# Performance work log

Hardware: AMD Instinct MI355X
Metric: run time of the kernel (lower is better)

Reference implementation:

```python
import jax, jax.numpy as jnp
import numpy as np

# Instant-NGP HashGrid constants (match tcnn encoding_config defaults in the module)
N_LEVELS = 16
N_FEATS = 2
LOG2_T = 16
T = 1 << LOG2_T            # hashmap entries per level
BASE_RES = 16
PER_LEVEL_SCALE = 1.5
N_POINTS = 1 << 20
PRIMES = (1, 2654435761, 805459861)  # tcnn spatial-hash primes

# 8 corner offsets of the unit cube, [8,3]
_CORNERS = np.array([[i, j, k] for i in (0, 1) for j in (0, 1) for k in (0, 1)], dtype=np.float32)


def setup_inputs() -> dict:
    key = jax.random.key(0)
    k1, k2 = jax.random.split(key)
    x = jax.random.uniform(k1, (N_POINTS, 3), dtype=jnp.float32)
    # tcnn initializes hash tables uniform in [-1e-4, 1e-4]
    table = jax.random.uniform(k2, (N_LEVELS, T, N_FEATS), minval=-1e-4, maxval=1e-4, dtype=jnp.float32)
    return {"x": x, "table": table}


def _corner_index(grid, res, dense):
    # grid: [N,8,3] int32 corner coordinates -> [N,8] table index
    if dense:
        g = jnp.clip(grid, 0, res - 1)
        return g[..., 0] + g[..., 1] * res + g[..., 2] * res * res
    g = grid.astype(jnp.uint32)
    h = (g[..., 0] * jnp.uint32(PRIMES[0])
         ^ g[..., 1] * jnp.uint32(PRIMES[1])
         ^ g[..., 2] * jnp.uint32(PRIMES[2]))
    return (h & jnp.uint32(T - 1)).astype(jnp.int32)


def _hashgrid_forward(x, table):
    x = x.astype(jnp.float32)
    offs = jnp.asarray(_CORNERS)                      # [8,3]
    outs = []
    for level in range(N_LEVELS):
        # tcnn: grid_scale = base * s^level - 1 ; resolution = ceil(scale)+1
        scale = float(BASE_RES * (PER_LEVEL_SCALE ** level) - 1.0)
        res = int(np.ceil(scale)) + 1
        dense = res ** 3 <= T                          # tcnn uses dense indexing when the grid fits
        pos = x * scale + 0.5                          # [N,3]
        g0 = jnp.floor(pos)
        frac = pos - g0                                # [N,3] trilinear fractions
        grid = (g0[:, None, :] + offs[None]).astype(jnp.int32)   # [N,8,3]
        idx = _corner_index(grid, res, dense)          # [N,8]
        feat = table[level][idx]                       # [N,8,F] irregular gather
        # trilinear weights: prod over dims of frac or (1-frac) per corner
        w = jnp.prod(jnp.where(offs[None] > 0, frac[:, None, :], 1.0 - frac[:, None, :]), axis=-1)  # [N,8]
        outs.append(jnp.sum(w[..., None] * feat, axis=1))        # [N,F]
    return jnp.concatenate(outs, axis=-1)              # [N, L*F] = [N,32]


def reference(x, table):
    return _hashgrid_forward(x, table)
```

## Files before the change

kernel.cpp:

```cpp
#include <hip/hip_runtime.h>
#include <stdint.h>


#define NLVL 16
#define TS 65536
#define P2 2654435761u
#define P3 805459861u

typedef float v4f __attribute__((ext_vector_type(4)));
typedef float v2f __attribute__((ext_vector_type(2)));
typedef float v4fa8 __attribute__((ext_vector_type(4), aligned(8)));

__constant__ float C_SCALES[NLVL] = {
    15.0f, 23.0f, 35.0f, 53.0f, 80.0f, 120.5f, 181.25f, 272.375f,
    409.0625f, 614.09375f, 921.640625f, 1382.9609375f,
    2074.94140625f, 3112.912109375f, 4669.8681640625f, 7005.30224609375f};

__device__ __forceinline__ v2f v4lo8(v4fa8 v) { v2f r; r.x = v.x; r.y = v.y; return r; }
__device__ __forceinline__ v2f v4hi8(v4fa8 v) { v2f r; r.x = v.z; r.y = v.w; return r; }

__device__ __forceinline__ void lds_put2(float* s, int p, int l,
                                         float a, float b) {
    const int t = l >> 3;
    const int gl = (l >> 1) & 3;
    const int slot = (gl + p) & 3;
    const int a32 = t * 4096 + p * 16 + slot * 4 + (l & 1) * 2;
    s[a32] = a;
    s[a32 + 1] = b;
}

struct LvlS {
    v2f c0, c1, c2, c3, c4, c5, c6, c7;
    float wx, wy, wz;
};

__device__ __forceinline__ void lvl_issue(LvlS& s, float px, float py,
                                          float pz, float scale,
                                          const v2f* __restrict__ tbl) {
    const float fx = px * scale + 0.5f;
    const float fy = py * scale + 0.5f;
    const float fz = pz * scale + 0.5f;
    const float gx = floorf(fx), gy = floorf(fy), gz = floorf(fz);
    s.wx = fx - gx;
    s.wy = fy - gy;
    s.wz = fz - gz;
    const uint32_t bx = (uint32_t)(int)gx, bx1 = bx + 1;
    const uint32_t hy0 = (uint32_t)(int)gy * P2, hy1 = hy0 + P2;
    const uint32_t hz0 = (uint32_t)(int)gz * P3, hz1 = hz0 + P3;
    const uint32_t b00 = hy0 ^ hz0, b01 = hy0 ^ hz1;
    const uint32_t b10 = hy1 ^ hz0, b11 = hy1 ^ hz1;
    s.c0 = tbl[(bx ^ b00) & (TS - 1)];
    s.c1 = tbl[(bx ^ b01) & (TS - 1)];
    s.c2 = tbl[(bx ^ b10) & (TS - 1)];
    s.c3 = tbl[(bx ^ b11) & (TS - 1)];
    s.c4 = tbl[(bx1 ^ b00) & (TS - 1)];
    s.c5 = tbl[(bx1 ^ b01) & (TS - 1)];
    s.c6 = tbl[(bx1 ^ b10) & (TS - 1)];
    s.c7 = tbl[(bx1 ^ b11) & (TS - 1)];
}

__device__ __forceinline__ v2f lvl_consume(const LvlS& s) {
    const float ux = 1.0f - s.wx, uy = 1.0f - s.wy, uz = 1.0f - s.wz;
    const float w0 = ux * uy * uz, w1 = ux * uy * s.wz;
    const float w2 = ux * s.wy * uz, w3 = ux * s.wy * s.wz;
    const float w4 = s.wx * uy * uz, w5 = s.wx * uy * s.wz;
    const float w6 = s.wx * s.wy * uz, w7 = s.wx * s.wy * s.wz;
    v2f o;
    o.x = w0 * s.c0.x + w1 * s.c1.x + w2 * s.c2.x + w3 * s.c3.x +
          w4 * s.c4.x + w5 * s.c5.x + w6 * s.c6.x + w7 * s.c7.x;
    o.y = w0 * s.c0.y + w1 * s.c1.y + w2 * s.c2.y + w3 * s.c3.y +
          w4 * s.c4.y + w5 * s.c5.y + w6 * s.c6.y + w7 * s.c7.y;
    return o;
}

__global__ __launch_bounds__(256, 4) void hashgrid_fwd(
    const float* __restrict__ x,
    const float* __restrict__ table,
    float* __restrict__ out,
    int n)
{
    __shared__ float s_out[256 * 32];

    const int tid0 = blockIdx.x * 256 + threadIdx.x;
    const int tid = min(tid0, n - 1);
    const int p = threadIdx.x;

    const float px = x[3 * tid + 0];
    const float py = x[3 * tid + 1];
    const float pz = x[3 * tid + 2];

    v4f* outb4 = (v4f*)out + (size_t)blockIdx.x * (256 * 8);
    const long long lim4 = (long long)n * 8 - (long long)blockIdx.x * (256 * 8);

    const v2f* tblv = (const v2f*)table;

    LvlS s0, s1, s2;
    lvl_issue(s0, px, py, pz, C_SCALES[3], tblv + (size_t)3 * TS);
    lvl_issue(s1, px, py, pz, C_SCALES[4], tblv + (size_t)4 * TS);
    lvl_issue(s2, px, py, pz, C_SCALES[5], tblv + (size_t)5 * TS);

    {
        const int RESO[3] = {16, 24, 36};
        const float DSC[3] = {15.0f, 23.0f, 35.0f};
#pragma unroll
        for (int l = 0; l < 3; ++l) {
            const float scale = DSC[l];
            const float fx = px * scale + 0.5f;
            const float fy = py * scale + 0.5f;
            const float fz = pz * scale + 0.5f;
            const float gx = floorf(fx), gy = floorf(fy), gz = floorf(fz);
            const float wx = fx - gx, wy = fy - gy, wz = fz - gz;
            const int ix = (int)gx, iy = (int)gy, iz = (int)gz;

            const v2f* tbl = tblv + (size_t)l * TS;
            const int R = RESO[l];
            const int x0 = min(ix, R - 1);
            const int y0 = min(iy, R - 1), y1 = min(iy + 1, R - 1);
            const int z0 = min(iz, R - 1), z1 = min(iz + 1, R - 1);
            const int xb = min(x0, R - 2);
            const bool hi0 = (x0 != xb);
            const int y0R = y0 * R, y1R = y1 * R;
            const int z0R = z0 * R * R, z1R = z1 * R * R;
            const v4fa8 f00 = *(const v4fa8*)(tbl + (xb + y0R + z0R));
            const v4fa8 f01 = *(const v4fa8*)(tbl + (xb + y0R + z1R));
            const v4fa8 f10 = *(const v4fa8*)(tbl + (xb + y1R + z0R));
            const v4fa8 f11 = *(const v4fa8*)(tbl + (xb + y1R + z1R));
            const v2f c0 = hi0 ? v4hi8(f00) : v4lo8(f00), c4 = v4hi8(f00);
            const v2f c1 = hi0 ? v4hi8(f01) : v4lo8(f01), c5 = v4hi8(f01);
            const v2f c2 = hi0 ? v4hi8(f10) : v4lo8(f10), c6 = v4hi8(f10);
            const v2f c3 = hi0 ? v4hi8(f11) : v4lo8(f11), c7 = v4hi8(f11);

            const float ux = 1.0f - wx, uy = 1.0f - wy, uz = 1.0f - wz;
            const float w0 = ux * uy * uz, w1 = ux * uy * wz;
            const float w2 = ux * wy * uz, w3 = ux * wy * wz;
            const float w4 = wx * uy * uz, w5 = wx * uy * wz;
            const float w6 = wx * wy * uz, w7 = wx * wy * wz;

            const float o0 = w0 * c0.x + w1 * c1.x + w2 * c2.x + w3 * c3.x +
                             w4 * c4.x + w5 * c5.x + w6 * c6.x + w7 * c7.x;
            const float o1 = w0 * c0.y + w1 * c1.y + w2 * c2.y + w3 * c3.y +
                             w4 * c4.y + w5 * c5.y + w6 * c6.y + w7 * c7.y;
            lds_put2(s_out, p, l, o0, o1);
        }
    }

#define STEP(S, LCUR) { const v2f o = lvl_consume(S); lds_put2(s_out, p, LCUR, o.x, o.y); }
#define REISSUE(S, LNXT) lvl_issue(S, px, py, pz, C_SCALES[LNXT], tblv + (size_t)(LNXT) * TS);

    STEP(s0, 3)  REISSUE(s0, 6)
    STEP(s1, 4)  REISSUE(s1, 7)
    STEP(s2, 5)  REISSUE(s2, 8)
    STEP(s0, 6)  REISSUE(s0, 9)
    STEP(s1, 7)  REISSUE(s1, 10)
    STEP(s2, 8)  REISSUE(s2, 11)
    STEP(s0, 9)  REISSUE(s0, 12)
    STEP(s1, 10) REISSUE(s1, 13)
    STEP(s2, 11) REISSUE(s2, 14)
    STEP(s0, 12) REISSUE(s0, 15)
    STEP(s1, 13)
    STEP(s2, 14)
    STEP(s0, 15)
#undef STEP
#undef REISSUE

    __syncthreads();

#pragma unroll
    for (int r = 0; r < 8; ++r) {
        const int e = r * 256 + threadIdx.x;
        const int pp = e >> 3, q = e & 7;
        const int t = q >> 2, g = q & 3;
        const int slot = (g + pp) & 3;
        const v4f v = *(const v4f*)&s_out[t * 4096 + pp * 16 + slot * 4];
        const int o4 = pp * 8 + q;
        if (o4 < lim4) outb4[o4] = v;
    }
}

extern "C" void kernel_launch(void* const* d_in, const int* in_sizes, int n_in,
                              void* d_out, int out_size, void* d_ws, size_t ws_size,
                              hipStream_t stream) {
    const float* x = (const float*)d_in[0];
    const float* table = (const float*)d_in[1];
    float* out = (float*)d_out;
    const int n = in_sizes[0] / 3;
    const int block = 256;
    const int grid = (n + block - 1) / block;
    hashgrid_fwd<<<grid, block, 0, stream>>>(x, table, out, n);
}
```

Baseline: 600.5 us.

## Halve LDS staging, drop to two in-flight levels, raise occupancy target

The output staging buffer is cut to half size and written out in two halves (levels 0-7, then 8-15), with extra barriers between them. The gather pipeline now keeps two levels in flight instead of three, and sched_barrier calls pin each issue group in place. Launch bounds go from 4 to 6 waves per EU so more blocks fit per CU and hide gather latency through parallelism. The cost is less memory-level parallelism per thread and extra synchronisation for the split writeback.

```diff
diff --git a/kernel.cpp b/kernel.cpp
--- a/kernel.cpp
+++ b/kernel.cpp
@@ -11,6 +11,8 @@
 typedef float v2f __attribute__((ext_vector_type(2)));
 typedef float v4fa8 __attribute__((ext_vector_type(4), aligned(8)));
 
+#define SB() __builtin_amdgcn_sched_barrier(0)
+
 __constant__ float C_SCALES[NLVL] = {
     15.0f, 23.0f, 35.0f, 53.0f, 80.0f, 120.5f, 181.25f, 272.375f,
     409.0625f, 614.09375f, 921.640625f, 1382.9609375f,
@@ -19,12 +21,10 @@
 __device__ __forceinline__ v2f v4lo8(v4fa8 v) { v2f r; r.x = v.x; r.y = v.y; return r; }
 __device__ __forceinline__ v2f v4hi8(v4fa8 v) { v2f r; r.x = v.z; r.y = v.w; return r; }
 
-__device__ __forceinline__ void lds_put2(float* s, int p, int l,
+__device__ __forceinline__ void lds_put2(float* s, int p, int gl, int h,
                                          float a, float b) {
-    const int t = l >> 3;
-    const int gl = (l >> 1) & 3;
     const int slot = (gl + p) & 3;
-    const int a32 = t * 4096 + p * 16 + slot * 4 + (l & 1) * 2;
+    const int a32 = p * 16 + slot * 4 + h * 2;
     s[a32] = a;
     s[a32 + 1] = b;
 }
@@ -73,13 +73,13 @@
     return o;
 }
 
-__global__ __launch_bounds__(256, 4) void hashgrid_fwd(
+__global__ __launch_bounds__(256, 6) void hashgrid_fwd(
     const float* __restrict__ x,
     const float* __restrict__ table,
     float* __restrict__ out,
     int n)
 {
-    __shared__ float s_out[256 * 32];
+    __shared__ float s_out[256 * 16];
 
     const int tid0 = blockIdx.x * 256 + threadIdx.x;
     const int tid = min(tid0, n - 1);
@@ -94,10 +94,16 @@
 
     const v2f* tblv = (const v2f*)table;
 
-    LvlS s0, s1, s2;
-    lvl_issue(s0, px, py, pz, C_SCALES[3], tblv + (size_t)3 * TS);
-    lvl_issue(s1, px, py, pz, C_SCALES[4], tblv + (size_t)4 * TS);
-    lvl_issue(s2, px, py, pz, C_SCALES[5], tblv + (size_t)5 * TS);
+#define STEP_H0(S, L) { const v2f o = lvl_consume(S); \
+                        lds_put2(s_out, p, (L) >> 1, (L) & 1, o.x, o.y); }
+#define STEP_H1(S, L) { const v2f o = lvl_consume(S); \
+                        lds_put2(s_out, p, ((L) >> 1) - 4, (L) & 1, o.x, o.y); }
+#define ISSUE(S, L) lvl_issue(S, px, py, pz, C_SCALES[L], \
+                              tblv + (size_t)(L) * TS); SB();
+
+    LvlS s0, s1;
+    ISSUE(s0, 3)
+    ISSUE(s1, 4)
 
     {
         const int RESO[3] = {16, 24, 36};
@@ -140,41 +146,51 @@
                              w4 * c4.x + w5 * c5.x + w6 * c6.x + w7 * c7.x;
             const float o1 = w0 * c0.y + w1 * c1.y + w2 * c2.y + w3 * c3.y +
                              w4 * c4.y + w5 * c5.y + w6 * c6.y + w7 * c7.y;
-            lds_put2(s_out, p, l, o0, o1);
+            lds_put2(s_out, p, l >> 1, l & 1, o0, o1);
         }
     }
 
-#define STEP(S, LCUR) { const v2f o = lvl_consume(S); lds_put2(s_out, p, LCUR, o.x, o.y); }
-#define REISSUE(S, LNXT) lvl_issue(S, px, py, pz, C_SCALES[LNXT], tblv + (size_t)(LNXT) * TS);
-
-    STEP(s0, 3)  REISSUE(s0, 6)
-    STEP(s1, 4)  REISSUE(s1, 7)
-    STEP(s2, 5)  REISSUE(s2, 8)
-    STEP(s0, 6)  REISSUE(s0, 9)
-    STEP(s1, 7)  REISSUE(s1, 10)
-    STEP(s2, 8)  REISSUE(s2, 11)
-    STEP(s0, 9)  REISSUE(s0, 12)
-    STEP(s1, 10) REISSUE(s1, 13)
-    STEP(s2, 11) REISSUE(s2, 14)
-    STEP(s0, 12) REISSUE(s0, 15)
-    STEP(s1, 13)
-    STEP(s2, 14)
-    STEP(s0, 15)
-#undef STEP
-#undef REISSUE
+    STEP_H0(s0, 3) ISSUE(s0, 5)
+    STEP_H0(s1, 4) ISSUE(s1, 6)
+    STEP_H0(s0, 5) ISSUE(s0, 7)
+    STEP_H0(s1, 6) ISSUE(s1, 8)
+    STEP_H0(s0, 7) ISSUE(s0, 9)
 
     __syncthreads();
-
 #pragma unroll
-    for (int r = 0; r < 8; ++r) {
+    for (int r = 0; r < 4; ++r) {
         const int e = r * 256 + threadIdx.x;
-        const int pp = e >> 3, q = e & 7;
-        const int t = q >> 2, g = q & 3;
+        const int pp = e >> 2, g = e & 3;
         const int slot = (g + pp) & 3;
-        const v4f v = *(const v4f*)&s_out[t * 4096 + pp * 16 + slot * 4];
-        const int o4 = pp * 8 + q;
+        const v4f v = *(const v4f*)&s_out[pp * 16 + slot * 4];
+        const int o4 = pp * 8 + g;
         if (o4 < lim4) outb4[o4] = v;
     }
+    __syncthreads();
+
+    STEP_H1(s1, 8)  ISSUE(s1, 10)
+    STEP_H1(s0, 9)  ISSUE(s0, 11)
+    STEP_H1(s1, 10) ISSUE(s1, 12)
+    STEP_H1(s0, 11) ISSUE(s0, 13)
+    STEP_H1(s1, 12) ISSUE(s1, 14)
+    STEP_H1(s0, 13) ISSUE(s0, 15)
+    STEP_H1(s1, 14)
+    STEP_H1(s0, 15)
+
+    __syncthreads();
+#pragma unroll
+    for (int r = 0; r < 4; ++r) {
+        const int e = r * 256 + threadIdx.x;
+        const int pp = e >> 2, g = e & 3;
+        const int slot = (g + pp) & 3;
+        const v4f v = *(const v4f*)&s_out[pp * 16 + slot * 4];
+        const int o4 = pp * 8 + 4 + g;
+        if (o4 < lim4) outb4[o4] = v;
+    }
+
+#undef STEP_H0
+#undef STEP_H1
+#undef ISSUE
 }
 
 extern "C" void kernel_launch(void* const* d_in, const int* in_sizes, int n_in,
```

New measurement: 659.3 us. 1.1x slower.
